# Optimization experiments

Measured on AMD Instinct MI355X. Metric: run time of the kernel, lower is better.

The kernel has to match this reference:

```python
import jax, jax.numpy as jnp
import numpy as np

N = 100000      # nodes
E = 1_600_000   # edges (avg degree 16)
IN, HID, OUT = 64, 64, 32


def setup_inputs() -> dict:
    key = jax.random.key(0)
    k1, k2, k3, k4, k5, k6 = jax.random.split(key, 6)
    x = jax.random.uniform(k1, (N, IN), dtype=jnp.float32)
    edge_index = jax.random.randint(k2, (2, E), 0, N, dtype=jnp.int32)
    # GCNConv weights (glorot-ish scale) and biases
    W1 = jax.random.normal(k3, (IN, HID), dtype=jnp.float32) * (1.0 / np.sqrt(IN))
    b1 = jnp.zeros((HID,), dtype=jnp.float32)
    W2 = jax.random.normal(k4, (HID, OUT), dtype=jnp.float32) * (1.0 / np.sqrt(HID))
    b2 = jnp.zeros((OUT,), dtype=jnp.float32)
    return {"x": x, "edge_index": edge_index, "W1": W1, "b1": b1, "W2": W2, "b2": b2}


def reference(x, edge_index, W1, b1, W2, b2):
    n = x.shape[0]
    # PyG GCNConv: add self-loops, symmetric deg^{-1/2} normalization
    loops = jnp.arange(n, dtype=edge_index.dtype)
    src = jnp.concatenate([edge_index[0], loops])  # message sources
    dst = jnp.concatenate([edge_index[1], loops])  # message targets
    ones = jnp.ones(src.shape[0], dtype=x.dtype)
    deg = jax.ops.segment_sum(ones, dst, num_segments=n)
    dinv = jnp.where(deg > 0, jax.lax.rsqrt(deg), 0.0)
    norm = dinv[src] * dinv[dst]  # [E+N]

    def gcn_conv(h, W, b):
        h = h @ W                          # [n, d_out]
        msg = h[src] * norm[:, None]       # gather + edge-normalize
        agg = jax.ops.segment_sum(msg, dst, num_segments=n)  # scatter-add
        return agg + b

    h = jax.nn.relu(gcn_conv(x, W1, b1))
    return gcn_conv(h, W2, b2)
```

## Files before the change

### kernel.cpp

```cpp
#include <hip/hip_runtime.h>
#include <hip/hip_fp16.h>


#define BSHIFT 7
#define BNODES 128
#define NB 256
#define NBINS 1024
#define CAP 2560

union H8 {
    uint4 u;
    __half2 h[4];
};

__device__ inline float2 u2f2(unsigned u) {
    union { unsigned x; __half2 h; } c;
    c.x = u;
    return __half22float2(c.h);
}
__device__ inline unsigned f2u(float a, float b) {
    union { unsigned x; __half2 h; } c;
    c.h = __floats2half2_rn(a, b);
    return c.x;
}

__global__ __launch_bounds__(256) void scatter_kernel(
    const int* __restrict__ src, const int* __restrict__ dst,
    int* __restrict__ cur, int* __restrict__ buf, int E) {
    __shared__ int h[NBINS];
    __shared__ int curl[NBINS];
    int t = threadIdx.x, b = blockIdx.x;
    for (int i = t; i < NBINS; i += 256) h[i] = 0;
    __syncthreads();
    int per = (E + NB - 1) / NB;
    int lo = b * per;
    int hi = min(lo + per, E);
    for (int i = lo + t; i < hi; i += 256) atomicAdd(&h[dst[i] >> BSHIFT], 1);
    __syncthreads();
    for (int i = t; i < NBINS; i += 256) {
        int c = h[i];
        curl[i] = c ? atomicAdd(&cur[i], c) : 0;
    }
    __syncthreads();
    for (int i = lo + t; i < hi; i += 256) {
        int d = dst[i];
        int bin = d >> BSHIFT;
        int loc = atomicAdd(&curl[bin], 1);
        if (loc < CAP)
            buf[(size_t)bin * CAP + loc] = (src[i] << BSHIFT) | (d & (BNODES - 1));
    }
}

__global__ __launch_bounds__(256) void bsort_kernel(
    const int* __restrict__ cur, int* __restrict__ buf,
    int2* __restrict__ off2, float* __restrict__ dinv, int N) {
    __shared__ int stage[CAP];
    __shared__ int h[BNODES];
    __shared__ int c2[BNODES];
    __shared__ int wtot;
    int t = threadIdx.x, b = blockIdx.x;
    int cnt = min(cur[b], CAP);
    int base = b * CAP;
    for (int i = t; i < cnt; i += 256) stage[i] = buf[base + i];
    if (t < BNODES) h[t] = 0;
    __syncthreads();
    for (int i = t; i < cnt; i += 256)
        atomicAdd(&h[stage[i] & (BNODES - 1)], 1);
    __syncthreads();
    int deg = (t < BNODES) ? h[t] : 0;
    int lane = t & 63;
    int v = deg;
#pragma unroll
    for (int d = 1; d < 64; d <<= 1) {
        int u = __shfl_up(v, d, 64);
        if (lane >= d) v += u;
    }
    if (t == 63) wtot = v;
    __syncthreads();
    if (t >= 64 && t < BNODES) v += wtot;
    int excl = v - deg;
    if (t < BNODES) {
        c2[t] = excl;
        int node = (b << BSHIFT) + t;
        if (node < N) {
            off2[node] = make_int2(base + excl, base + excl + deg);
            dinv[node] = rsqrtf((float)(deg + 1));
        }
    }
    __syncthreads();
    for (int i = t; i < cnt; i += 256) {
        int p = stage[i];
        int pos = atomicAdd(&c2[p & (BNODES - 1)], 1);
        buf[base + pos] = p >> BSHIFT;
    }
}

__global__ __launch_bounds__(256) void gemm1_kernel(
    const float* __restrict__ x, const float* __restrict__ W1,
    const float* __restrict__ dinv, __half* __restrict__ hsh, int N) {
    __shared__ float4 Ws[64 * 16];
    int t = threadIdx.x;
    const float4* W4 = (const float4*)W1;
    for (int i = t; i < 1024; i += 256) Ws[i] = W4[i];
    __syncthreads();
    int c = t & 3;
    int rg = t >> 2;
    int r0 = blockIdx.x * 256 + rg * 4;
    if (r0 >= N) return;
    int nm1 = N - 1;
    float4 acc[4][4];
#pragma unroll
    for (int r = 0; r < 4; r++)
#pragma unroll
        for (int j = 0; j < 4; j++) acc[r][j] = make_float4(0.f, 0.f, 0.f, 0.f);
    const float4* x4 = (const float4*)x;
    for (int k4 = 0; k4 < 16; k4++) {
        float4 xv[4];
#pragma unroll
        for (int r = 0; r < 4; r++)
            xv[r] = x4[(size_t)min(r0 + r, nm1) * 16 + k4];
#pragma unroll
        for (int kk = 0; kk < 4; kk++) {
            const float4* wr = &Ws[(k4 * 4 + kk) * 16 + c * 4];
            float4 w0 = wr[0], w1 = wr[1], w2 = wr[2], w3 = wr[3];
#pragma unroll
            for (int r = 0; r < 4; r++) {
                float a = (kk == 0) ? xv[r].x : (kk == 1) ? xv[r].y
                          : (kk == 2) ? xv[r].z : xv[r].w;
                acc[r][0].x += a * w0.x; acc[r][0].y += a * w0.y;
                acc[r][0].z += a * w0.z; acc[r][0].w += a * w0.w;
                acc[r][1].x += a * w1.x; acc[r][1].y += a * w1.y;
                acc[r][1].z += a * w1.z; acc[r][1].w += a * w1.w;
                acc[r][2].x += a * w2.x; acc[r][2].y += a * w2.y;
                acc[r][2].z += a * w2.z; acc[r][2].w += a * w2.w;
                acc[r][3].x += a * w3.x; acc[r][3].y += a * w3.y;
                acc[r][3].z += a * w3.z; acc[r][3].w += a * w3.w;
            }
        }
    }
#pragma unroll
    for (int r = 0; r < 4; r++) {
        int row = r0 + r;
        if (row >= N) break;
        float di = dinv[row];
        uint4* ha = (uint4*)(hsh + (size_t)row * 64);
        H8 p0, p1;
        p0.h[0] = __floats2half2_rn(acc[r][0].x * di, acc[r][0].y * di);
        p0.h[1] = __floats2half2_rn(acc[r][0].z * di, acc[r][0].w * di);
        p0.h[2] = __floats2half2_rn(acc[r][1].x * di, acc[r][1].y * di);
        p0.h[3] = __floats2half2_rn(acc[r][1].z * di, acc[r][1].w * di);
        p1.h[0] = __floats2half2_rn(acc[r][2].x * di, acc[r][2].y * di);
        p1.h[1] = __floats2half2_rn(acc[r][2].z * di, acc[r][2].w * di);
        p1.h[2] = __floats2half2_rn(acc[r][3].x * di, acc[r][3].y * di);
        p1.h[3] = __floats2half2_rn(acc[r][3].z * di, acc[r][3].w * di);
        ha[c * 2 + 0] = p0.u;
        ha[c * 2 + 1] = p1.u;
    }
}

__global__ __launch_bounds__(256) void agg1gemm2_kernel(
    const uint4* __restrict__ hsh4, const int* __restrict__ ssrc,
    const int2* __restrict__ off2, const float* __restrict__ dinv,
    const float* __restrict__ b1, const float* __restrict__ W2,
    __half* __restrict__ gsh, int N) {
    __shared__ float4 Ws2[64 * 8];
    int t = threadIdx.x;
    const float4* W24 = (const float4*)W2;
    for (int i = t; i < 512; i += 256) Ws2[i] = W24[i];
    __syncthreads();
    int lane = t & 63;
    int wid = (blockIdx.x * 256 + t) >> 6;
    int node = wid * 8 + (lane >> 3);
    int fi = lane & 7;
    if (node >= N) return;
    int2 lh = off2[node];
    int lo = lh.x, hi = lh.y;
    float di = dinv[node];
    H8 sv;
    sv.u = hsh4[(size_t)node * 8 + fi];
    float2 a0 = __half22float2(sv.h[0]);
    float2 a1 = __half22float2(sv.h[1]);
    float2 a2 = __half22float2(sv.h[2]);
    float2 a3 = __half22float2(sv.h[3]);
    float2 c0 = make_float2(0.f, 0.f), c1 = make_float2(0.f, 0.f);
    float2 c2 = make_float2(0.f, 0.f), c3 = make_float2(0.f, 0.f);
    int hm1 = hi - 1;
    for (int e = lo; e < hi; e += 8) {
        int i1 = min(e + 1, hm1), i2 = min(e + 2, hm1), i3 = min(e + 3, hm1);
        int i4 = min(e + 4, hm1), i5 = min(e + 5, hm1), i6 = min(e + 6, hm1),
            i7 = min(e + 7, hm1);
        int s0 = __builtin_nontemporal_load(&ssrc[e]);
        int s1 = __builtin_nontemporal_load(&ssrc[i1]);
        int s2 = __builtin_nontemporal_load(&ssrc[i2]);
        int s3 = __builtin_nontemporal_load(&ssrc[i3]);
        int s4 = __builtin_nontemporal_load(&ssrc[i4]);
        int s5 = __builtin_nontemporal_load(&ssrc[i5]);
        int s6 = __builtin_nontemporal_load(&ssrc[i6]);
        int s7 = __builtin_nontemporal_load(&ssrc[i7]);
        H8 v0, v1, v2, v3, v4, v5, v6, v7;
        v0.u = hsh4[(size_t)s0 * 8 + fi];
        v1.u = hsh4[(size_t)s1 * 8 + fi];
        v2.u = hsh4[(size_t)s2 * 8 + fi];
        v3.u = hsh4[(size_t)s3 * 8 + fi];
        v4.u = hsh4[(size_t)s4 * 8 + fi];
        v5.u = hsh4[(size_t)s5 * 8 + fi];
        v6.u = hsh4[(size_t)s6 * 8 + fi];
        v7.u = hsh4[(size_t)s7 * 8 + fi];
        float m1 = (e + 1 < hi) ? 1.f : 0.f;
        float m2 = (e + 2 < hi) ? 1.f : 0.f;
        float m3 = (e + 3 < hi) ? 1.f : 0.f;
        float m4 = (e + 4 < hi) ? 1.f : 0.f;
        float m5 = (e + 5 < hi) ? 1.f : 0.f;
        float m6 = (e + 6 < hi) ? 1.f : 0.f;
        float m7 = (e + 7 < hi) ? 1.f : 0.f;
#pragma unroll
        for (int q = 0; q < 4; q++) {
            float2* aA = (q == 0) ? &a0 : (q == 1) ? &a1 : (q == 2) ? &a2 : &a3;
            float2* cA = (q == 0) ? &c0 : (q == 1) ? &c1 : (q == 2) ? &c2 : &c3;
            float2 f0 = __half22float2(v0.h[q]);
            float2 f1 = __half22float2(v1.h[q]);
            float2 f2 = __half22float2(v2.h[q]);
            float2 f3 = __half22float2(v3.h[q]);
            float2 f4 = __half22float2(v4.h[q]);
            float2 f5 = __half22float2(v5.h[q]);
            float2 f6 = __half22float2(v6.h[q]);
            float2 f7 = __half22float2(v7.h[q]);
            aA->x += f0.x + m1 * f1.x + m2 * f2.x + m3 * f3.x;
            aA->y += f0.y + m1 * f1.y + m2 * f2.y + m3 * f3.y;
            cA->x += m4 * f4.x + m5 * f5.x + m6 * f6.x + m7 * f7.x;
            cA->y += m4 * f4.y + m5 * f5.y + m6 * f6.y + m7 * f7.y;
        }
    }
    float4 bl = ((const float4*)b1)[fi * 2];
    float4 bh = ((const float4*)b1)[fi * 2 + 1];
    float r0 = fmaxf((a0.x + c0.x) * di + bl.x, 0.f);
    float r1 = fmaxf((a0.y + c0.y) * di + bl.y, 0.f);
    float r2 = fmaxf((a1.x + c1.x) * di + bl.z, 0.f);
    float r3 = fmaxf((a1.y + c1.y) * di + bl.w, 0.f);
    float r4 = fmaxf((a2.x + c2.x) * di + bh.x, 0.f);
    float r5 = fmaxf((a2.y + c2.y) * di + bh.y, 0.f);
    float r6 = fmaxf((a3.x + c3.x) * di + bh.z, 0.f);
    float r7 = fmaxf((a3.y + c3.y) * di + bh.w, 0.f);
    unsigned pk0 = f2u(r0, r1), pk1 = f2u(r2, r3);
    unsigned pk2 = f2u(r4, r5), pk3 = f2u(r6, r7);
    float4 acc2 = make_float4(0.f, 0.f, 0.f, 0.f);
#pragma unroll
    for (int s = 0; s < 8; s++) {
        int sl = (fi + s) & 7;
        unsigned u0 = __shfl(pk0, sl, 8);
        unsigned u1 = __shfl(pk1, sl, 8);
        unsigned u2 = __shfl(pk2, sl, 8);
        unsigned u3 = __shfl(pk3, sl, 8);
        float2 f0 = u2f2(u0), f1 = u2f2(u1), f2 = u2f2(u2), f3 = u2f2(u3);
        const float4* wr = &Ws2[sl * 64 + fi];
        float4 w;
        w = wr[0];
        acc2.x += f0.x * w.x; acc2.y += f0.x * w.y;
        acc2.z += f0.x * w.z; acc2.w += f0.x * w.w;
        w = wr[8];
        acc2.x += f0.y * w.x; acc2.y += f0.y * w.y;
        acc2.z += f0.y * w.z; acc2.w += f0.y * w.w;
        w = wr[16];
        acc2.x += f1.x * w.x; acc2.y += f1.x * w.y;
        acc2.z += f1.x * w.z; acc2.w += f1.x * w.w;
        w = wr[24];
        acc2.x += f1.y * w.x; acc2.y += f1.y * w.y;
        acc2.z += f1.y * w.z; acc2.w += f1.y * w.w;
        w = wr[32];
        acc2.x += f2.x * w.x; acc2.y += f2.x * w.y;
        acc2.z += f2.x * w.z; acc2.w += f2.x * w.w;
        w = wr[40];
        acc2.x += f2.y * w.x; acc2.y += f2.y * w.y;
        acc2.z += f2.y * w.z; acc2.w += f2.y * w.w;
        w = wr[48];
        acc2.x += f3.x * w.x; acc2.y += f3.x * w.y;
        acc2.z += f3.x * w.z; acc2.w += f3.x * w.w;
        w = wr[56];
        acc2.x += f3.y * w.x; acc2.y += f3.y * w.y;
        acc2.z += f3.y * w.z; acc2.w += f3.y * w.w;
    }
    uint2 pg;
    pg.x = f2u(acc2.x * di, acc2.y * di);
    pg.y = f2u(acc2.z * di, acc2.w * di);
    ((uint2*)gsh)[(size_t)node * 8 + fi] = pg;
}

__global__ __launch_bounds__(256) void agg2_kernel(
    const uint4* __restrict__ gsh4, const int* __restrict__ ssrc,
    const int2* __restrict__ off2, const float* __restrict__ dinv,
    const float* __restrict__ b2, float4* __restrict__ out4, int N) {
    int lane = threadIdx.x & 63;
    int wid = (blockIdx.x * 256 + threadIdx.x) >> 6;
    int node = wid * 16 + (lane >> 2);
    int fi = lane & 3;
    if (node >= N) return;
    int2 lh = off2[node];
    int lo = lh.x, hi = lh.y;
    float di = dinv[node];
    H8 sv;
    sv.u = gsh4[(size_t)node * 4 + fi];
    float2 a0 = __half22float2(sv.h[0]);
    float2 a1 = __half22float2(sv.h[1]);
    float2 a2 = __half22float2(sv.h[2]);
    float2 a3 = __half22float2(sv.h[3]);
    float2 c0 = make_float2(0.f, 0.f), c1 = make_float2(0.f, 0.f);
    float2 c2 = make_float2(0.f, 0.f), c3 = make_float2(0.f, 0.f);
    int hm1 = hi - 1;
    for (int e = lo; e < hi; e += 8) {
        int i1 = min(e + 1, hm1), i2 = min(e + 2, hm1), i3 = min(e + 3, hm1);
        int i4 = min(e + 4, hm1), i5 = min(e + 5, hm1), i6 = min(e + 6, hm1),
            i7 = min(e + 7, hm1);
        int s0 = __builtin_nontemporal_load(&ssrc[e]);
        int s1 = __builtin_nontemporal_load(&ssrc[i1]);
        int s2 = __builtin_nontemporal_load(&ssrc[i2]);
        int s3 = __builtin_nontemporal_load(&ssrc[i3]);
        int s4 = __builtin_nontemporal_load(&ssrc[i4]);
        int s5 = __builtin_nontemporal_load(&ssrc[i5]);
        int s6 = __builtin_nontemporal_load(&ssrc[i6]);
        int s7 = __builtin_nontemporal_load(&ssrc[i7]);
        H8 v0, v1, v2, v3, v4, v5, v6, v7;
        v0.u = gsh4[(size_t)s0 * 4 + fi];
        v1.u = gsh4[(size_t)s1 * 4 + fi];
        v2.u = gsh4[(size_t)s2 * 4 + fi];
        v3.u = gsh4[(size_t)s3 * 4 + fi];
        v4.u = gsh4[(size_t)s4 * 4 + fi];
        v5.u = gsh4[(size_t)s5 * 4 + fi];
        v6.u = gsh4[(size_t)s6 * 4 + fi];
        v7.u = gsh4[(size_t)s7 * 4 + fi];
        float m1 = (e + 1 < hi) ? 1.f : 0.f;
        float m2 = (e + 2 < hi) ? 1.f : 0.f;
        float m3 = (e + 3 < hi) ? 1.f : 0.f;
        float m4 = (e + 4 < hi) ? 1.f : 0.f;
        float m5 = (e + 5 < hi) ? 1.f : 0.f;
        float m6 = (e + 6 < hi) ? 1.f : 0.f;
        float m7 = (e + 7 < hi) ? 1.f : 0.f;
#pragma unroll
        for (int q = 0; q < 4; q++) {
            float2* aA = (q == 0) ? &a0 : (q == 1) ? &a1 : (q == 2) ? &a2 : &a3;
            float2* cA = (q == 0) ? &c0 : (q == 1) ? &c1 : (q == 2) ? &c2 : &c3;
            float2 f0 = __half22float2(v0.h[q]);
            float2 f1 = __half22float2(v1.h[q]);
            float2 f2 = __half22float2(v2.h[q]);
            float2 f3 = __half22float2(v3.h[q]);
            float2 f4 = __half22float2(v4.h[q]);
            float2 f5 = __half22float2(v5.h[q]);
            float2 f6 = __half22float2(v6.h[q]);
            float2 f7 = __half22float2(v7.h[q]);
            aA->x += f0.x + m1 * f1.x + m2 * f2.x + m3 * f3.x;
            aA->y += f0.y + m1 * f1.y + m2 * f2.y + m3 * f3.y;
            cA->x += m4 * f4.x + m5 * f5.x + m6 * f6.x + m7 * f7.x;
            cA->y += m4 * f4.y + m5 * f5.y + m6 * f6.y + m7 * f7.y;
        }
    }
    float4 bl = ((const float4*)b2)[fi * 2];
    float4 bh = ((const float4*)b2)[fi * 2 + 1];
    float4 r0, r1;
    r0.x = (a0.x + c0.x) * di + bl.x;
    r0.y = (a0.y + c0.y) * di + bl.y;
    r0.z = (a1.x + c1.x) * di + bl.z;
    r0.w = (a1.y + c1.y) * di + bl.w;
    r1.x = (a2.x + c2.x) * di + bh.x;
    r1.y = (a2.y + c2.y) * di + bh.y;
    r1.z = (a3.x + c3.x) * di + bh.z;
    r1.w = (a3.y + c3.y) * di + bh.w;
    out4[(size_t)node * 8 + fi * 2 + 0] = r0;
    out4[(size_t)node * 8 + fi * 2 + 1] = r1;
}

extern "C" void kernel_launch(void* const* d_in, const int* in_sizes, int n_in,
                              void* d_out, int out_size, void* d_ws,
                              size_t ws_size, hipStream_t stream) {
    const float* x  = (const float*)d_in[0];
    const int* ei   = (const int*)d_in[1];
    const float* W1 = (const float*)d_in[2];
    const float* b1 = (const float*)d_in[3];
    const float* W2 = (const float*)d_in[4];
    const float* b2 = (const float*)d_in[5];
    int N = in_sizes[0] / 64;
    int E = in_sizes[1] / 2;
    const int* src = ei;
    const int* dst = ei + E;
    int B = (N + BNODES - 1) >> BSHIFT;

    char* ws = (char*)d_ws;
    size_t o = 0;
    auto align16 = [&o]() { o = (o + 15) & ~(size_t)15; };
    int* cur    = (int*)(ws + o); o += NBINS * 4; align16();
    int* buf    = (int*)(ws + o); o += (size_t)B * CAP * 4; align16();
    int2* off2  = (int2*)(ws + o); o += (size_t)N * 8; align16();
    float* dinv = (float*)(ws + o); o += (size_t)N * 4; align16();
    __half* hsh = (__half*)(ws + o); o += (size_t)N * 64 * 2; align16();
    __half* gsh = (__half*)(ws + o); o += (size_t)N * 32 * 2; align16();
    float* outp = (float*)d_out;

    hipMemsetAsync(cur, 0, NBINS * 4, stream);
    scatter_kernel<<<NB, 256, 0, stream>>>(src, dst, cur, buf, E);
    bsort_kernel<<<B, 256, 0, stream>>>(cur, buf, off2, dinv, N);
    gemm1_kernel<<<(N + 255) / 256, 256, 0, stream>>>(x, W1, dinv, hsh, N);
    agg1gemm2_kernel<<<(N + 31) / 32, 256, 0, stream>>>(
        (const uint4*)hsh, buf, off2, dinv, b1, W2, gsh, N);
    agg2_kernel<<<(N + 63) / 64, 256, 0, stream>>>(
        (const uint4*)gsh, buf, off2, dinv, b2, (float4*)outp, N);
}
```

Before: 207.2 us.

## Stage edges in shared memory per block before coalesced bucket writes

The scatter kernel now computes a local prefix sum over its per-bin histogram, places each edge into a shared-memory buffer sorted by bin, and then copies each bin's run to global memory with groups of 8 threads writing consecutive positions. Before, each edge was written straight to a scattered global slot. The aim is to turn random global stores into mostly contiguous ones. The cost is an extra shared-memory pass, a block scan, and about 25KB more LDS per block, which could lower occupancy.

Result: slower. 224.7 us (+8.4%).

```diff
diff --git a/kernel.cpp b/kernel.cpp
--- a/kernel.cpp
+++ b/kernel.cpp
@@ -5,7 +5,8 @@
 #define BSHIFT 7
 #define BNODES 128
 #define NB 256
-#define NBINS 1024
+#define PER_MAX 6250
+#define PBINS 1024
 #define CAP 2560
 
 union H8 {
@@ -27,27 +28,70 @@
 __global__ __launch_bounds__(256) void scatter_kernel(
     const int* __restrict__ src, const int* __restrict__ dst,
     int* __restrict__ cur, int* __restrict__ buf, int E) {
-    __shared__ int h[NBINS];
-    __shared__ int curl[NBINS];
+    __shared__ int sorted[PER_MAX];
+    __shared__ int hist[PBINS];
+    __shared__ int lbase[PBINS];
+    __shared__ int curs[PBINS];
+    __shared__ int gbase[PBINS];
+    __shared__ int wtot[4];
     int t = threadIdx.x, b = blockIdx.x;
-    for (int i = t; i < NBINS; i += 256) h[i] = 0;
-    __syncthreads();
     int per = (E + NB - 1) / NB;
     int lo = b * per;
     int hi = min(lo + per, E);
-    for (int i = lo + t; i < hi; i += 256) atomicAdd(&h[dst[i] >> BSHIFT], 1);
-    __syncthreads();
-    for (int i = t; i < NBINS; i += 256) {
-        int c = h[i];
-        curl[i] = c ? atomicAdd(&cur[i], c) : 0;
-    }
+    for (int i = t; i < PBINS; i += 256) hist[i] = 0;
+    __syncthreads();
+    for (int i = lo + t; i < hi; i += 256)
+        atomicAdd(&hist[dst[i] >> BSHIFT], 1);
+    __syncthreads();
+    int tb = t * 4;
+    int h0 = hist[tb], h1 = hist[tb + 1], h2 = hist[tb + 2], h3 = hist[tb + 3];
+    int s = h0 + h1 + h2 + h3;
+    int lane = t & 63;
+    int v = s;
+#pragma unroll
+    for (int d = 1; d < 64; d <<= 1) {
+        int u = __shfl_up(v, d, 64);
+        if (lane >= d) v += u;
+    }
+    if (lane == 63) wtot[t >> 6] = v;
+    __syncthreads();
+    int woff = 0;
+    int wv = t >> 6;
+#pragma unroll
+    for (int w = 0; w < 4; w++)
+        if (w < wv) woff += wtot[w];
+    int excl = woff + v - s;
+    lbase[tb + 0] = excl;
+    lbase[tb + 1] = excl + h0;
+    lbase[tb + 2] = excl + h0 + h1;
+    lbase[tb + 3] = excl + h0 + h1 + h2;
+    curs[tb + 0] = lbase[tb + 0];
+    curs[tb + 1] = lbase[tb + 1];
+    curs[tb + 2] = lbase[tb + 2];
+    curs[tb + 3] = lbase[tb + 3];
+    gbase[tb + 0] = h0 ? atomicAdd(&cur[tb + 0], h0) : 0;
+    gbase[tb + 1] = h1 ? atomicAdd(&cur[tb + 1], h1) : 0;
+    gbase[tb + 2] = h2 ? atomicAdd(&cur[tb + 2], h2) : 0;
+    gbase[tb + 3] = h3 ? atomicAdd(&cur[tb + 3], h3) : 0;
     __syncthreads();
     for (int i = lo + t; i < hi; i += 256) {
         int d = dst[i];
         int bin = d >> BSHIFT;
-        int loc = atomicAdd(&curl[bin], 1);
-        if (loc < CAP)
-            buf[(size_t)bin * CAP + loc] = (src[i] << BSHIFT) | (d & (BNODES - 1));
+        int pos = atomicAdd(&curs[bin], 1);
+        sorted[pos] = (src[i] << BSHIFT) | (d & (BNODES - 1));
+    }
+    __syncthreads();
+    int bg = t >> 3, sub = t & 7;
+    for (int bin = bg; bin < PBINS; bin += 32) {
+        int c = hist[bin];
+        if (c == 0) continue;
+        int lb = lbase[bin];
+        int g = gbase[bin];
+        size_t obase = (size_t)bin * CAP;
+        for (int j = sub; j < c; j += 8) {
+            int p = g + j;
+            if (p < CAP) buf[obase + p] = sorted[lb + j];
+        }
     }
 }
 
@@ -385,7 +429,7 @@
     char* ws = (char*)d_ws;
     size_t o = 0;
     auto align16 = [&o]() { o = (o + 15) & ~(size_t)15; };
-    int* cur    = (int*)(ws + o); o += NBINS * 4; align16();
+    int* cur    = (int*)(ws + o); o += PBINS * 4; align16();
     int* buf    = (int*)(ws + o); o += (size_t)B * CAP * 4; align16();
     int2* off2  = (int2*)(ws + o); o += (size_t)N * 8; align16();
     float* dinv = (float*)(ws + o); o += (size_t)N * 4; align16();
@@ -393,7 +437,7 @@
     __half* gsh = (__half*)(ws + o); o += (size_t)N * 32 * 2; align16();
     float* outp = (float*)d_out;
 
-    hipMemsetAsync(cur, 0, NBINS * 4, stream);
+    hipMemsetAsync(cur, 0, PBINS * 4, stream);
     scatter_kernel<<<NB, 256, 0, stream>>>(src, dst, cur, buf, E);
     bsort_kernel<<<B, 256, 0, stream>>>(cur, buf, off2, dinv, N);
     gemm1_kernel<<<(N + 255) / 256, 256, 0, stream>>>(x, W1, dinv, hsh, N);
```
